# Performance work log

Measured on AMD Instinct MI355X. Metric: run time of the kernel, lower is better.

Reference implementation:

```python
import jax, jax.numpy as jnp
import numpy as np

D_MODEL = 1024
D_STATE = 16
D_CONV = 4
EXPAND = 2
NUM_LAYERS = 2
SEQ = 1024
BATCH = 2
D_INNER = EXPAND * D_MODEL          # 2048
DT_RANK = (D_MODEL + 15) // 16      # 64 (math.ceil(d_model/16))


def setup_inputs() -> dict:
    key = jax.random.key(0)
    ks = jax.random.split(key, 10)
    s = 0.02
    # A initialized as in mamba_ssm: A = repeat(arange(1, d_state+1), d_inner) -> A_log = log(A)
    A_log = jnp.log(jnp.broadcast_to(
        jnp.arange(1, D_STATE + 1, dtype=jnp.float32), (NUM_LAYERS, D_INNER, D_STATE)))
    return {
        "pe": jax.random.normal(ks[0], (SEQ, D_MODEL), jnp.float32) * s,
        "condition": jax.random.normal(ks[1], (BATCH, SEQ, D_MODEL), jnp.float32),
        "W_in": jax.random.normal(ks[2], (NUM_LAYERS, 2 * D_INNER, D_MODEL), jnp.float32) * s,
        "conv_w": jax.random.normal(ks[3], (NUM_LAYERS, D_INNER, D_CONV), jnp.float32) * s,
        "conv_b": jnp.zeros((NUM_LAYERS, D_INNER), jnp.float32),
        "W_x": jax.random.normal(ks[4], (NUM_LAYERS, DT_RANK + 2 * D_STATE, D_INNER), jnp.float32) * s,
        "W_dt": jax.random.normal(ks[5], (NUM_LAYERS, D_INNER, DT_RANK), jnp.float32) * s,
        "b_dt": jax.random.normal(ks[6], (NUM_LAYERS, D_INNER), jnp.float32) * s,
        "A_log": A_log,
        "Dp": jnp.ones((NUM_LAYERS, D_INNER), jnp.float32),
        "W_out": jax.random.normal(ks[7], (NUM_LAYERS, D_MODEL, D_INNER), jnp.float32) * s,
        "output_shape": BATCH,
    }


def _mamba_block(x, W_in, conv_w, conv_b, W_x, W_dt, b_dt, A_log, Dp, W_out):
    # x: [B, L, d_model]
    B, L, _ = x.shape
    xz = jnp.einsum('bld,ed->ble', x, W_in)          # [B, L, 2*d_inner]
    u, z = jnp.split(xz, 2, axis=-1)                 # each [B, L, d_inner]
    # causal depthwise conv1d (padding=d_conv-1, truncate to L)
    xp = jnp.pad(u, ((0, 0), (D_CONV - 1, 0), (0, 0)))
    xc = conv_b + sum(conv_w[:, k] * xp[:, k:k + L, :] for k in range(D_CONV))
    xc = jax.nn.silu(xc)                             # [B, L, d_inner]
    x_dbl = jnp.einsum('bld,ed->ble', xc, W_x)       # [B, L, dt_rank + 2*d_state]
    dt, Bm, Cm = jnp.split(x_dbl, [DT_RANK, DT_RANK + D_STATE], axis=-1)
    delta = jax.nn.softplus(jnp.einsum('blr,dr->bld', dt, W_dt) + b_dt)  # [B, L, d_inner]
    A = -jnp.exp(A_log)                              # [d_inner, d_state]

    def step(h, inputs):
        u_t, d_t, B_t, C_t = inputs                  # [B,di],[B,di],[B,ds],[B,ds]
        dA = jnp.exp(d_t[:, :, None] * A)            # [B, di, ds]
        h = dA * h + (d_t * u_t)[:, :, None] * B_t[:, None, :]
        y = jnp.einsum('bds,bs->bd', h, C_t)
        return h, y

    h0 = jnp.zeros((B, D_INNER, D_STATE), x.dtype)
    xs = (xc.transpose(1, 0, 2), delta.transpose(1, 0, 2),
          Bm.transpose(1, 0, 2), Cm.transpose(1, 0, 2))
    _, ys = jax.lax.scan(step, h0, xs)               # ys: [L, B, d_inner]
    y = ys.transpose(1, 0, 2) + xc * Dp
    out = y * jax.nn.silu(z)
    return jnp.einsum('bld,ed->ble', out, W_out)     # [B, L, d_model]


def reference(pe, condition, W_in, conv_w, conv_b, W_x, W_dt, b_dt, A_log, Dp, W_out, output_shape):
    # pe.repeat(B,1,1) + condition
    x = pe[None, :, :] + condition
    for i in range(NUM_LAYERS):
        x = _mamba_block(x, W_in[i], conv_w[i], conv_b[i], W_x[i],
                         W_dt[i], b_dt[i], A_log[i], Dp[i], W_out[i])
    return x
```

## Files before the change

kernel.cpp:

```cpp
#include <hip/hip_runtime.h>
#include <math.h>

#define D_MODEL 1024
#define D_INNER 2048
#define D_STATE 16
#define DT_RANK 64
#define SEQ 1024
#define BATCH 2
#define NLAYERS 2
#define ROWS (BATCH*SEQ)
#define XDIM 96
#define XZLD (2*D_INNER)

#define NC 32
#define CL 32
#define SDB 256

#define G2_ROWS 64
#define G2_KC 128
#define G2_BK 32
#define G2_KS (D_INNER / G2_KC)

typedef short bf16x8 __attribute__((ext_vector_type(8)));
typedef float f32x4  __attribute__((ext_vector_type(4)));

__device__ __forceinline__ unsigned short f2bf(float f) {
    union { float f; unsigned int u; } v; v.f = f;
    unsigned int u = v.u;
    return (unsigned short)((u + 0x7FFFu + ((u >> 16) & 1u)) >> 16);
}
__device__ __forceinline__ float bf2f(unsigned short u) {
    union { unsigned int i; float f; } v; v.i = ((unsigned int)u) << 16; return v.f;
}

__device__ __forceinline__ void gload_lds16(const void* g, void* s) {
    __builtin_amdgcn_global_load_lds((const __attribute__((address_space(1))) void*)g,
                                     (__attribute__((address_space(3))) void*)s, 16, 0, 0);
}

__global__ __launch_bounds__(256) void add_pe_kernel(const float* __restrict__ pe,
    const float* __restrict__ cond, float* __restrict__ X)
{
    int i = blockIdx.x * 256 + threadIdx.x;
    int total = ROWS * D_MODEL / 4;
    if (i >= total) return;
    int row  = i / (D_MODEL / 4);
    int l    = row & (SEQ - 1);
    int col4 = i - row * (D_MODEL / 4);
    float4 p = reinterpret_cast<const float4*>(pe)[l * (D_MODEL / 4) + col4];
    float4 c = reinterpret_cast<const float4*>(cond)[i];
    float4 r; r.x = p.x + c.x; r.y = p.y + c.y; r.z = p.z + c.z; r.w = p.w + c.w;
    reinterpret_cast<float4*>(X)[i] = r;
}

__global__ __launch_bounds__(256) void add_pe_bf(const float* __restrict__ pe,
    const float* __restrict__ cond, unsigned short* __restrict__ Xbf)
{
    int i = blockIdx.x * 256 + threadIdx.x;
    int total = ROWS * D_MODEL / 4;
    if (i >= total) return;
    int row  = i / (D_MODEL / 4);
    int l    = row & (SEQ - 1);
    int col4 = i - row * (D_MODEL / 4);
    float4 p = reinterpret_cast<const float4*>(pe)[l * (D_MODEL / 4) + col4];
    float4 c = reinterpret_cast<const float4*>(cond)[i];
    ushort4 o;
    o.x = f2bf(p.x + c.x); o.y = f2bf(p.y + c.y);
    o.z = f2bf(p.z + c.z); o.w = f2bf(p.w + c.w);
    reinterpret_cast<ushort4*>(Xbf)[i] = o;
}

__global__ __launch_bounds__(256) void conv_bf16_dense(const float* __restrict__ src,
    unsigned short* __restrict__ dst, int n4)
{
    int i = blockIdx.x * 256 + threadIdx.x;
    if (i >= n4) return;
    float4 v = reinterpret_cast<const float4*>(src)[i];
    ushort4 o; o.x = f2bf(v.x); o.y = f2bf(v.y); o.z = f2bf(v.z); o.w = f2bf(v.w);
    reinterpret_cast<ushort4*>(dst)[i] = o;
}

__global__ __launch_bounds__(256) void conv_bf16_strided(const float* __restrict__ src,
    int ld, int cols, unsigned short* __restrict__ dst, int total4)
{
    int i = blockIdx.x * 256 + threadIdx.x;
    if (i >= total4) return;
    int c4  = cols / 4;
    int row = i / c4;
    int col = (i - row * c4) * 4;
    float4 v = *reinterpret_cast<const float4*>(src + (size_t)row * ld + col);
    ushort4 o; o.x = f2bf(v.x); o.y = f2bf(v.y); o.z = f2bf(v.z); o.w = f2bf(v.w);
    *reinterpret_cast<ushort4*>(dst + (size_t)row * cols + col) = o;
}

__global__ __launch_bounds__(256) void conv_bf16_dtcols(const float* __restrict__ XDBL,
    unsigned short* __restrict__ dst)
{
    int i = blockIdx.x * 256 + threadIdx.x;
    if (i >= ROWS * DT_RANK / 4) return;
    int m  = i >> 4;
    int c4 = (i & 15) * 4;
    float4 v = *reinterpret_cast<const float4*>(XDBL + (size_t)m * XDIM + c4);
    ushort4 o; o.x = f2bf(v.x); o.y = f2bf(v.y); o.z = f2bf(v.z); o.w = f2bf(v.w);
    *reinterpret_cast<ushort4*>(dst + (size_t)m * DT_RANK + c4) = o;
}

#define GBM 128
#define GBN 128
#define GBK 64

#define GEMM_STAGE(Ap, Bp, lda, ldb, koff)                                      \
    _Pragma("unroll")                                                           \
    for (int i_ = 0; i_ < 4; ++i_) {                                            \
        int off_ = w * 4096 + i_ * 1024 + l * 16;                               \
        int row_ = off_ >> 7;                                                   \
        int col_ = (off_ & 127) >> 1;                                           \
        gload_lds16(Ap + (size_t)(m0 + row_) * (lda) + (koff) + col_,           \
                    (char*)As + w * 4096 + i_ * 1024);                          \
    }                                                                           \
    _Pragma("unroll")                                                           \
    for (int i_ = 0; i_ < 4; ++i_) {                                            \
        int off_ = w * 4096 + i_ * 1024 + l * 16;                               \
        int row_ = off_ >> 7;                                                   \
        int col_ = (off_ & 127) >> 1;                                           \
        gload_lds16(Bp + (size_t)(n0 + row_) * (ldb) + (koff) + col_,           \
                    (char*)Bs + w * 4096 + i_ * 1024);                          \
    }

#define GEMM_MFMA_STEP                                                          \
    _Pragma("unroll")                                                           \
    for (int kk = 0; kk < 2; ++kk) {                                            \
        bf16x8 af[4], bfr[4];                                                   \
        _Pragma("unroll")                                                       \
        for (int m = 0; m < 4; ++m)                                             \
            af[m] = *(const bf16x8*)&As[(wr * 64 + m * 16 + fr) * GBK + kk * 32 + fq * 8]; \
        _Pragma("unroll")                                                       \
        for (int n = 0; n < 4; ++n)                                             \
            bfr[n] = *(const bf16x8*)&Bs[(wc * 64 + n * 16 + fr) * GBK + kk * 32 + fq * 8]; \
        _Pragma("unroll")                                                       \
        for (int m = 0; m < 4; ++m)                                             \
            _Pragma("unroll")                                                   \
            for (int n = 0; n < 4; ++n)                                         \
                acc[m][n] = __builtin_amdgcn_mfma_f32_16x16x32_bf16(af[m], bfr[n], acc[m][n], 0, 0, 0); \
    }

__global__ __launch_bounds__(256) void gemm_bf16_nt(const unsigned short* __restrict__ A,
    const unsigned short* __restrict__ B, float* __restrict__ C,
    int M, int N, int K, int ldc, const float* __restrict__ bias, int epilogue)
{
    __shared__ unsigned short As[GBM * GBK];
    __shared__ unsigned short Bs[GBN * GBK];
    int tid = threadIdx.x;
    int w = tid >> 6, l = tid & 63;
    int wr = w >> 1, wc = w & 1;
    int m0 = blockIdx.y * GBM, n0 = blockIdx.x * GBN;

    f32x4 acc[4][4];
    #pragma unroll
    for (int m = 0; m < 4; ++m)
        #pragma unroll
        for (int n = 0; n < 4; ++n) acc[m][n] = (f32x4){0.f, 0.f, 0.f, 0.f};
    int fr = l & 15, fq = l >> 4;

    for (int k0 = 0; k0 < K; k0 += GBK) {
        GEMM_STAGE(A, B, K, K, k0)
        __syncthreads();
        GEMM_MFMA_STEP
        __syncthreads();
    }

    #pragma unroll
    for (int m = 0; m < 4; ++m)
        #pragma unroll
        for (int n = 0; n < 4; ++n) {
            int col = n0 + wc * 64 + n * 16 + fr;
            #pragma unroll
            for (int j = 0; j < 4; ++j) {
                int row = m0 + wr * 64 + m * 16 + fq * 4 + j;
                float v = acc[m][n][j];
                if (epilogue == 1) {
                    v += bias[col];
                    v = fmaxf(v, 0.f) + log1pf(__expf(-fabsf(v)));
                }
                C[(size_t)row * ldc + col] = v;
            }
        }
}

__global__ __launch_bounds__(256) void gemm_bf16_nt_bfout(const unsigned short* __restrict__ A,
    const unsigned short* __restrict__ B, unsigned short* __restrict__ C,
    int M, int N, int K, int ldc)
{
    __shared__ unsigned short As[GBM * GBK];
    __shared__ unsigned short Bs[GBN * GBK];
    int tid = threadIdx.x;
    int w = tid >> 6, l = tid & 63;
    int wr = w >> 1, wc = w & 1;
    int m0 = blockIdx.y * GBM, n0 = blockIdx.x * GBN;

    f32x4 acc[4][4];
    #pragma unroll
    for (int m = 0; m < 4; ++m)
        #pragma unroll
        for (int n = 0; n < 4; ++n) acc[m][n] = (f32x4){0.f, 0.f, 0.f, 0.f};
    int fr = l & 15, fq = l >> 4;

    for (int k0 = 0; k0 < K; k0 += GBK) {
        GEMM_STAGE(A, B, K, K, k0)
        __syncthreads();
        GEMM_MFMA_STEP
        __syncthreads();
    }

    #pragma unroll
    for (int m = 0; m < 4; ++m)
        #pragma unroll
        for (int n = 0; n < 4; ++n) {
            int col = n0 + wc * 64 + n * 16 + fr;
            #pragma unroll
            for (int j = 0; j < 4; ++j) {
                int row = m0 + wr * 64 + m * 16 + fq * 4 + j;
                C[(size_t)row * ldc + col] = f2bf(acc[m][n][j]);
            }
        }
}

__global__ __launch_bounds__(256) void gemm_bf16_sp_bfout(const unsigned short* __restrict__ A,
    const unsigned short* __restrict__ B, unsigned short* __restrict__ C,
    int M, int N, int K, int ldc, const float* __restrict__ bias)
{
    __shared__ unsigned short As[GBM * GBK];
    __shared__ unsigned short Bs[GBN * GBK];
    int tid = threadIdx.x;
    int w = tid >> 6, l = tid & 63;
    int wr = w >> 1, wc = w & 1;
    int m0 = blockIdx.y * GBM, n0 = blockIdx.x * GBN;

    f32x4 acc[4][4];
    #pragma unroll
    for (int m = 0; m < 4; ++m)
        #pragma unroll
        for (int n = 0; n < 4; ++n) acc[m][n] = (f32x4){0.f, 0.f, 0.f, 0.f};
    int fr = l & 15, fq = l >> 4;

    for (int k0 = 0; k0 < K; k0 += GBK) {
        GEMM_STAGE(A, B, K, K, k0)
        __syncthreads();
        GEMM_MFMA_STEP
        __syncthreads();
    }

    #pragma unroll
    for (int m = 0; m < 4; ++m)
        #pragma unroll
        for (int n = 0; n < 4; ++n) {
            int col = n0 + wc * 64 + n * 16 + fr;
            float bv = bias[col];
            #pragma unroll
            for (int j = 0; j < 4; ++j) {
                int row = m0 + wr * 64 + m * 16 + fq * 4 + j;
                float v = acc[m][n][j] + bv;
                v = fmaxf(v, 0.f) + log1pf(__expf(-fabsf(v)));
                C[(size_t)row * ldc + col] = f2bf(v);
            }
        }
}

__global__ __launch_bounds__(256) void gemm_bf16_nt_ks(const unsigned short* __restrict__ A, int lda,
    const unsigned short* __restrict__ B, int ldb, float* __restrict__ P,
    int M, int N, int Kper)
{
    __shared__ unsigned short As[GBM * GBK];
    __shared__ unsigned short Bs[GBN * GBK];
    int tid = threadIdx.x;
    int w = tid >> 6, l = tid & 63;
    int wr = w >> 1, wc = w & 1;
    int m0 = blockIdx.y * GBM, n0 = blockIdx.x * GBN;
    int koff = blockIdx.z * Kper;
    float* Pz = P + (size_t)blockIdx.z * M * N;

    f32x4 acc[4][4];
    #pragma unroll
    for (int m = 0; m < 4; ++m)
        #pragma unroll
        for (int n = 0; n < 4; ++n) acc[m][n] = (f32x4){0.f, 0.f, 0.f, 0.f};
    int fr = l & 15, fq = l >> 4;

    for (int k0 = 0; k0 < Kper; k0 += GBK) {
        GEMM_STAGE(A, B, lda, ldb, koff + k0)
        __syncthreads();
        GEMM_MFMA_STEP
        __syncthreads();
    }

    #pragma unroll
    for (int m = 0; m < 4; ++m)
        #pragma unroll
        for (int n = 0; n < 4; ++n) {
            int col = n0 + wc * 64 + n * 16 + fr;
            #pragma unroll
            for (int j = 0; j < 4; ++j) {
                int row = m0 + wr * 64 + m * 16 + fq * 4 + j;
                Pz[(size_t)row * N + col] = acc[m][n][j];
            }
        }
}

__global__ __launch_bounds__(256) void gemm4_reduce(const float* __restrict__ P,
    float* __restrict__ X, unsigned short* __restrict__ Xbf)
{
    int i = blockIdx.x * 256 + threadIdx.x;
    if (i >= ROWS * D_MODEL / 4) return;
    float4 a = reinterpret_cast<const float4*>(P)[i];
    float4 b = reinterpret_cast<const float4*>(P + (size_t)ROWS * D_MODEL)[i];
    float4 r; r.x = a.x + b.x; r.y = a.y + b.y; r.z = a.z + b.z; r.w = a.w + b.w;
    if (X) reinterpret_cast<float4*>(X)[i] = r;
    if (Xbf) {
        ushort4 o; o.x = f2bf(r.x); o.y = f2bf(r.y); o.z = f2bf(r.z); o.w = f2bf(r.w);
        reinterpret_cast<ushort4*>(Xbf)[i] = o;
    }
}

__global__ __launch_bounds__(256) void gemm2_splitk(const float* __restrict__ A,
    const float* __restrict__ B, float* __restrict__ P)
{
    __shared__ float As[G2_BK][G2_ROWS];
    __shared__ float Bs[G2_BK][XDIM + 1];
    int tid = threadIdx.x;
    int m0 = blockIdx.x * G2_ROWS;
    int kc = blockIdx.y;
    int k0 = kc * G2_KC;

    int rg = tid >> 4;
    int cg = tid & 15;
    float acc[4][6];
    #pragma unroll
    for (int i = 0; i < 4; ++i)
        #pragma unroll
        for (int j = 0; j < 6; ++j) acc[i][j] = 0.f;

    for (int kb = 0; kb < G2_KC; kb += G2_BK) {
        {
            int row = tid & 63;
            int kk  = (tid >> 6) * 4;
            #pragma unroll
            for (int i = 0; i < 2; ++i) {
                float4 v = *(const float4*)(A + (size_t)(m0 + row) * D_INNER + k0 + kb + kk + i * 16);
                As[kk + i * 16 + 0][row] = v.x;
                As[kk + i * 16 + 1][row] = v.y;
                As[kk + i * 16 + 2][row] = v.z;
                As[kk + i * 16 + 3][row] = v.w;
            }
        }
        {
            #pragma unroll
            for (int i = 0; i < 3; ++i) {
                int idx = tid + i * 256;
                int col = idx >> 3;
                int kk  = (idx & 7) * 4;
                float4 v = *(const float4*)(B + (size_t)col * D_INNER + k0 + kb + kk);
                Bs[kk + 0][col] = v.x;
                Bs[kk + 1][col] = v.y;
                Bs[kk + 2][col] = v.z;
                Bs[kk + 3][col] = v.w;
            }
        }
        __syncthreads();
        #pragma unroll
        for (int k = 0; k < G2_BK; ++k) {
            float4 a  = *(const float4*)&As[k][rg * 4];
            float2 b0 = *(const float2*)&Bs[k][cg * 6];
            float2 b1 = *(const float2*)&Bs[k][cg * 6 + 2];
            float2 b2 = *(const float2*)&Bs[k][cg * 6 + 4];
            float av[4] = {a.x, a.y, a.z, a.w};
            float bv[6] = {b0.x, b0.y, b1.x, b1.y, b2.x, b2.y};
            #pragma unroll
            for (int i = 0; i < 4; ++i)
                #pragma unroll
                for (int j = 0; j < 6; ++j) acc[i][j] += av[i] * bv[j];
        }
        __syncthreads();
    }

    #pragma unroll
    for (int i = 0; i < 4; ++i)
        #pragma unroll
        for (int j = 0; j < 6; ++j)
            P[((size_t)kc * ROWS + m0 + rg * 4 + i) * XDIM + cg * 6 + j] = acc[i][j];
}

__global__ __launch_bounds__(256) void gemm2_reduce(const float* __restrict__ P,
    float* __restrict__ XDBLo, unsigned short* __restrict__ dtbf)
{
    int i = blockIdx.x * 256 + threadIdx.x;
    if (i >= ROWS * XDIM / 4) return;
    float4 acc = make_float4(0.f, 0.f, 0.f, 0.f);
    #pragma unroll
    for (int ks = 0; ks < G2_KS; ++ks) {
        float4 v = *(const float4*)(P + (size_t)ks * ROWS * XDIM + (size_t)i * 4);
        acc.x += v.x; acc.y += v.y; acc.z += v.z; acc.w += v.w;
    }
    *(float4*)(XDBLo + (size_t)i * 4) = acc;
    if (dtbf) {
        int row = (i * 4) / XDIM;
        int col = (i * 4) - row * XDIM;
        if (col < DT_RANK) {
            ushort4 o; o.x = f2bf(acc.x); o.y = f2bf(acc.y); o.z = f2bf(acc.z); o.w = f2bf(acc.w);
            *reinterpret_cast<ushort4*>(dtbf + (size_t)row * DT_RANK + col) = o;
        }
    }
}

#define BM 64
#define BN 64
#define BK 16
__global__ __launch_bounds__(256) void gemm_nt(const float* __restrict__ A, int lda,
                                               const float* __restrict__ B, int ldb,
                                               float* __restrict__ C, int ldc,
                                               int M, int N, int K,
                                               const float* __restrict__ bias, int epilogue)
{
    __shared__ float As[BM][BK + 1];
    __shared__ float Bs[BN][BK + 1];
    int t  = threadIdx.x;
    int m0 = blockIdx.y * BM;
    int n0 = blockIdx.x * BN;
    int lrow = t >> 2;
    int lk   = (t & 3) * 4;
    int tm   = t >> 4;
    int tn   = t & 15;

    float acc[4][4];
    #pragma unroll
    for (int i = 0; i < 4; ++i)
        #pragma unroll
        for (int j = 0; j < 4; ++j) acc[i][j] = 0.f;

    for (int k0 = 0; k0 < K; k0 += BK) {
        {
            int row = m0 + lrow;
            float4 v = make_float4(0.f, 0.f, 0.f, 0.f);
            if (row < M) v = *reinterpret_cast<const float4*>(A + (size_t)row * lda + k0 + lk);
            As[lrow][lk + 0] = v.x; As[lrow][lk + 1] = v.y;
            As[lrow][lk + 2] = v.z; As[lrow][lk + 3] = v.w;
        }
        {
            int row = n0 + lrow;
            float4 v = make_float4(0.f, 0.f, 0.f, 0.f);
            if (row < N) v = *reinterpret_cast<const float4*>(B + (size_t)row * ldb + k0 + lk);
            Bs[lrow][lk + 0] = v.x; Bs[lrow][lk + 1] = v.y;
            Bs[lrow][lk + 2] = v.z; Bs[lrow][lk + 3] = v.w;
        }
        __syncthreads();
        #pragma unroll
        for (int kk = 0; kk < BK; ++kk) {
            float a[4], b[4];
            #pragma unroll
            for (int i = 0; i < 4; ++i) a[i] = As[tm * 4 + i][kk];
            #pragma unroll
            for (int j = 0; j < 4; ++j) b[j] = Bs[tn * 4 + j][kk];
            #pragma unroll
            for (int i = 0; i < 4; ++i)
                #pragma unroll
                for (int j = 0; j < 4; ++j) acc[i][j] += a[i] * b[j];
        }
        __syncthreads();
    }

    #pragma unroll
    for (int i = 0; i < 4; ++i) {
        int m = m0 + tm * 4 + i;
        if (m >= M) continue;
        #pragma unroll
        for (int j = 0; j < 4; ++j) {
            int n = n0 + tn * 4 + j;
            if (n >= N) continue;
            float v = acc[i][j];
            if (epilogue == 1) {
                v += bias[n];
                v = fmaxf(v, 0.f) + log1pf(__expf(-fabsf(v)));
            }
            C[(size_t)m * ldc + n] = v;
        }
    }
}

__global__ __launch_bounds__(256) void conv_silu_kernel(const float* __restrict__ XZ,
    const float* __restrict__ cw, const float* __restrict__ cb, float* __restrict__ XC)
{
    int idx = blockIdx.x * 256 + threadIdx.x;
    if (idx >= ROWS * (D_INNER / 4)) return;
    int d4   = idx % (D_INNER / 4);
    int rl   = idx / (D_INNER / 4);
    int l    = rl & (SEQ - 1);
    int base = rl - l;
    int d    = d4 * 4;

    float4 acc = reinterpret_cast<const float4*>(cb)[d4];
    float w[4][4];
    #pragma unroll
    for (int dd = 0; dd < 4; ++dd) {
        float4 wv = *reinterpret_cast<const float4*>(cw + (size_t)(d + dd) * 4);
        w[dd][0] = wv.x; w[dd][1] = wv.y; w[dd][2] = wv.z; w[dd][3] = wv.w;
    }
    #pragma unroll
    for (int k = 0; k < 4; ++k) {
        int lr = l - 3 + k;
        if (lr < 0) continue;
        float4 u = *reinterpret_cast<const float4*>(XZ + (size_t)(base + lr) * XZLD + d);
        acc.x += w[0][k] * u.x; acc.y += w[1][k] * u.y;
        acc.z += w[2][k] * u.z; acc.w += w[3][k] * u.w;
    }
    acc.x = acc.x / (1.f + __expf(-acc.x));
    acc.y = acc.y / (1.f + __expf(-acc.y));
    acc.z = acc.z / (1.f + __expf(-acc.z));
    acc.w = acc.w / (1.f + __expf(-acc.w));
    reinterpret_cast<float4*>(XC)[idx] = acc;
}

__global__ __launch_bounds__(256) void conv_silu_bf(const unsigned short* __restrict__ XZbf,
    const float* __restrict__ cw, const float* __restrict__ cb, float* __restrict__ XC)
{
    int idx = blockIdx.x * 256 + threadIdx.x;
    if (idx >= ROWS * (D_INNER / 4)) return;
    int d4   = idx % (D_INNER / 4);
    int rl   = idx / (D_INNER / 4);
    int l    = rl & (SEQ - 1);
    int base = rl - l;
    int d    = d4 * 4;

    float4 acc = reinterpret_cast<const float4*>(cb)[d4];
    float w[4][4];
    #pragma unroll
    for (int dd = 0; dd < 4; ++dd) {
        float4 wv = *reinterpret_cast<const float4*>(cw + (size_t)(d + dd) * 4);
        w[dd][0] = wv.x; w[dd][1] = wv.y; w[dd][2] = wv.z; w[dd][3] = wv.w;
    }
    #pragma unroll
    for (int k = 0; k < 4; ++k) {
        int lr = l - 3 + k;
        if (lr < 0) continue;
        ushort4 uv = *reinterpret_cast<const ushort4*>(XZbf + (size_t)(base + lr) * XZLD + d);
        acc.x += w[0][k] * bf2f(uv.x); acc.y += w[1][k] * bf2f(uv.y);
        acc.z += w[2][k] * bf2f(uv.z); acc.w += w[3][k] * bf2f(uv.w);
    }
    acc.x = acc.x / (1.f + __expf(-acc.x));
    acc.y = acc.y / (1.f + __expf(-acc.y));
    acc.z = acc.z / (1.f + __expf(-acc.z));
    acc.w = acc.w / (1.f + __expf(-acc.w));
    reinterpret_cast<float4*>(XC)[idx] = acc;
}


__global__ __launch_bounds__(SDB) void scan_part1b(const float* __restrict__ XC,
    const unsigned short* __restrict__ DL, const float* __restrict__ XDBL,
    const float* __restrict__ A_log, float* __restrict__ Psum, float* __restrict__ Ssum)
{
    __shared__ float sB[CL][16];
    int tid = threadIdx.x;
    int d = blockIdx.x * SDB + tid;
    int c = blockIdx.y, b = blockIdx.z;
    size_t r0 = (size_t)b * SEQ + (size_t)c * CL;

    if (tid < CL * 4) {
        int t = tid >> 2, j = (tid & 3) * 4;
        *(float4*)&sB[t][j] = *(const float4*)(XDBL + (r0 + t) * XDIM + DT_RANK + j);
    }

    float a[D_STATE], S[D_STATE];
    #pragma unroll
    for (int i = 0; i < 4; ++i) {
        float4 v = *(const float4*)(A_log + (size_t)d * D_STATE + i * 4);
        a[i*4+0] = -__expf(v.x); a[i*4+1] = -__expf(v.y);
        a[i*4+2] = -__expf(v.z); a[i*4+3] = -__expf(v.w);
    }
    #pragma unroll
    for (int s = 0; s < D_STATE; ++s) S[s] = 0.f;
    float sumdl = 0.f;
    __syncthreads();

    for (int t = 0; t < CL; ++t) {
        float dl = bf2f(DL[(r0 + t) * D_INNER + d]);
        float uu = XC[(r0 + t) * D_INNER + d];
        float du = dl * uu;
        sumdl += dl;
        float4 b0 = *(const float4*)&sB[t][0];
        float4 b1 = *(const float4*)&sB[t][4];
        float4 b2 = *(const float4*)&sB[t][8];
        float4 b3 = *(const float4*)&sB[t][12];
        float bv[16] = {b0.x,b0.y,b0.z,b0.w, b1.x,b1.y,b1.z,b1.w,
                        b2.x,b2.y,b2.z,b2.w, b3.x,b3.y,b3.z,b3.w};
        #pragma unroll
        for (int s = 0; s < D_STATE; ++s) {
            float e = __expf(dl * a[s]);
            S[s] = e * S[s] + du * bv[s];
        }
    }

    size_t o = (((size_t)b * NC + c) * D_INNER + d) * D_STATE;
    #pragma unroll
    for (int i = 0; i < 4; ++i) {
        float4 p, s4;
        p.x = __expf(a[i*4+0] * sumdl); p.y = __expf(a[i*4+1] * sumdl);
        p.z = __expf(a[i*4+2] * sumdl); p.w = __expf(a[i*4+3] * sumdl);
        s4.x = S[i*4+0]; s4.y = S[i*4+1]; s4.z = S[i*4+2]; s4.w = S[i*4+3];
        *(float4*)(Psum + o + i * 4) = p;
        *(float4*)(Ssum + o + i * 4) = s4;
    }
}

__global__ __launch_bounds__(256) void scan_prefix(float* __restrict__ Psum,
    const float* __restrict__ Ssum)
{
    int idx = blockIdx.x * 256 + threadIdx.x;
    int b = idx >> 15;
    int rem = idx & 32767;
    float h = 0.f;
    for (int c = 0; c < NC; ++c) {
        size_t o = (((size_t)b * NC + c) * D_INNER * D_STATE) + rem;
        float p = Psum[o];
        float s = Ssum[o];
        Psum[o] = h;
        h = p * h + s;
    }
}

__global__ __launch_bounds__(SDB) void scan_part2b(const float* __restrict__ XC,
    unsigned short* __restrict__ DL, const unsigned short* __restrict__ XZbf,
    const float* __restrict__ XDBL, const float* __restrict__ A_log,
    const float* __restrict__ Dp, const float* __restrict__ Hin)
{
    __shared__ float sBC[CL][32];
    int tid = threadIdx.x;
    int d = blockIdx.x * SDB + tid;
    int c = blockIdx.y, b = blockIdx.z;
    size_t r0 = (size_t)b * SEQ + (size_t)c * CL;

    {
        int t = tid >> 3, j = (tid & 7) * 4;
        *(float4*)&sBC[t][j] = *(const float4*)(XDBL + (r0 + t) * XDIM + DT_RANK + j);
    }

    float a[D_STATE], h[D_STATE];
    #pragma unroll
    for (int i = 0; i < 4; ++i) {
        float4 v = *(const float4*)(A_log + (size_t)d * D_STATE + i * 4);
        a[i*4+0] = -__expf(v.x); a[i*4+1] = -__expf(v.y);
        a[i*4+2] = -__expf(v.z); a[i*4+3] = -__expf(v.w);
    }
    size_t ho = (((size_t)b * NC + c) * D_INNER + d) * D_STATE;
    #pragma unroll
    for (int i = 0; i < 4; ++i) {
        float4 v = *(const float4*)(Hin + ho + i * 4);
        h[i*4+0] = v.x; h[i*4+1] = v.y; h[i*4+2] = v.z; h[i*4+3] = v.w;
    }
    float dp = Dp[d];
    __syncthreads();

    for (int t = 0; t < CL; ++t) {
        float dl = bf2f(DL[(r0 + t) * D_INNER + d]);
        float uu = XC[(r0 + t) * D_INNER + d];
        float z  = bf2f(XZbf[(r0 + t) * XZLD + D_INNER + d]);
        float du = dl * uu;
        float4 b0 = *(const float4*)&sBC[t][0];
        float4 b1 = *(const float4*)&sBC[t][4];
        float4 b2 = *(const float4*)&sBC[t][8];
        float4 b3 = *(const float4*)&sBC[t][12];
        float4 c0 = *(const float4*)&sBC[t][16];
        float4 c1 = *(const float4*)&sBC[t][20];
        float4 c2 = *(const float4*)&sBC[t][24];
        float4 c3 = *(const float4*)&sBC[t][28];
        float bv[16] = {b0.x,b0.y,b0.z,b0.w, b1.x,b1.y,b1.z,b1.w,
                        b2.x,b2.y,b2.z,b2.w, b3.x,b3.y,b3.z,b3.w};
        float cv[16] = {c0.x,c0.y,c0.z,c0.w, c1.x,c1.y,c1.z,c1.w,
                        c2.x,c2.y,c2.z,c2.w, c3.x,c3.y,c3.z,c3.w};
        float y = 0.f;
        #pragma unroll
        for (int s = 0; s < D_STATE; ++s) {
            float e = __expf(dl * a[s]);
            h[s] = e * h[s] + du * bv[s];
            y += h[s] * cv[s];
        }
        float sz = z / (1.f + __expf(-z));
        DL[(r0 + t) * D_INNER + d] = f2bf((y + uu * dp) * sz);
    }
}

__global__ __launch_bounds__(SDB) void scan_part1(const float* __restrict__ XC,
    const float* __restrict__ XZ, const float* __restrict__ XDBL,
    const float* __restrict__ A_log, float* __restrict__ Psum, float* __restrict__ Ssum)
{
    __shared__ float sB[CL][16];
    int tid = threadIdx.x;
    int d = blockIdx.x * SDB + tid;
    int c = blockIdx.y, b = blockIdx.z;
    size_t r0 = (size_t)b * SEQ + (size_t)c * CL;

    if (tid < CL * 4) {
        int t = tid >> 2, j = (tid & 3) * 4;
        *(float4*)&sB[t][j] = *(const float4*)(XDBL + (r0 + t) * XDIM + DT_RANK + j);
    }

    float a[D_STATE], S[D_STATE];
    #pragma unroll
    for (int i = 0; i < 4; ++i) {
        float4 v = *(const float4*)(A_log + (size_t)d * D_STATE + i * 4);
        a[i*4+0] = -__expf(v.x); a[i*4+1] = -__expf(v.y);
        a[i*4+2] = -__expf(v.z); a[i*4+3] = -__expf(v.w);
    }
    #pragma unroll
    for (int s = 0; s < D_STATE; ++s) S[s] = 0.f;
    float sumdl = 0.f;
    __syncthreads();

    for (int t = 0; t < CL; ++t) {
        float dl = XZ[(r0 + t) * XZLD + d];
        float uu = XC[(r0 + t) * D_INNER + d];
        float du = dl * uu;
        sumdl += dl;
        float4 b0 = *(const float4*)&sB[t][0];
        float4 b1 = *(const float4*)&sB[t][4];
        float4 b2 = *(const float4*)&sB[t][8];
        float4 b3 = *(const float4*)&sB[t][12];
        float bv[16] = {b0.x,b0.y,b0.z,b0.w, b1.x,b1.y,b1.z,b1.w,
                        b2.x,b2.y,b2.z,b2.w, b3.x,b3.y,b3.z,b3.w};
        #pragma unroll
        for (int s = 0; s < D_STATE; ++s) {
            float e = __expf(dl * a[s]);
            S[s] = e * S[s] + du * bv[s];
        }
    }

    size_t o = (((size_t)b * NC + c) * D_INNER + d) * D_STATE;
    #pragma unroll
    for (int i = 0; i < 4; ++i) {
        float4 p, s4;
        p.x = __expf(a[i*4+0] * sumdl); p.y = __expf(a[i*4+1] * sumdl);
        p.z = __expf(a[i*4+2] * sumdl); p.w = __expf(a[i*4+3] * sumdl);
        s4.x = S[i*4+0]; s4.y = S[i*4+1]; s4.z = S[i*4+2]; s4.w = S[i*4+3];
        *(float4*)(Psum + o + i * 4) = p;
        *(float4*)(Ssum + o + i * 4) = s4;
    }
}

__global__ __launch_bounds__(SDB) void scan_part2(const float* __restrict__ XC,
    float* __restrict__ XZ, const float* __restrict__ XDBL,
    const float* __restrict__ A_log, const float* __restrict__ Dp,
    const float* __restrict__ Hin)
{
    __shared__ float sBC[CL][32];
    int tid = threadIdx.x;
    int d = blockIdx.x * SDB + tid;
    int c = blockIdx.y, b = blockIdx.z;
    size_t r0 = (size_t)b * SEQ + (size_t)c * CL;

    {
        int t = tid >> 3, j = (tid & 7) * 4;
        *(float4*)&sBC[t][j] = *(const float4*)(XDBL + (r0 + t) * XDIM + DT_RANK + j);
    }

    float a[D_STATE], h[D_STATE];
    #pragma unroll
    for (int i = 0; i < 4; ++i) {
        float4 v = *(const float4*)(A_log + (size_t)d * D_STATE + i * 4);
        a[i*4+0] = -__expf(v.x); a[i*4+1] = -__expf(v.y);
        a[i*4+2] = -__expf(v.z); a[i*4+3] = -__expf(v.w);
    }
    size_t ho = (((size_t)b * NC + c) * D_INNER + d) * D_STATE;
    #pragma unroll
    for (int i = 0; i < 4; ++i) {
        float4 v = *(const float4*)(Hin + ho + i * 4);
        h[i*4+0] = v.x; h[i*4+1] = v.y; h[i*4+2] = v.z; h[i*4+3] = v.w;
    }
    float dp = Dp[d];
    __syncthreads();

    for (int t = 0; t < CL; ++t) {
        float dl = XZ[(r0 + t) * XZLD + d];
        float uu = XC[(r0 + t) * D_INNER + d];
        float z  = XZ[(r0 + t) * XZLD + D_INNER + d];
        float du = dl * uu;
        float4 b0 = *(const float4*)&sBC[t][0];
        float4 b1 = *(const float4*)&sBC[t][4];
        float4 b2 = *(const float4*)&sBC[t][8];
        float4 b3 = *(const float4*)&sBC[t][12];
        float4 c0 = *(const float4*)&sBC[t][16];
        float4 c1 = *(const float4*)&sBC[t][20];
        float4 c2 = *(const float4*)&sBC[t][24];
        float4 c3 = *(const float4*)&sBC[t][28];
        float bv[16] = {b0.x,b0.y,b0.z,b0.w, b1.x,b1.y,b1.z,b1.w,
                        b2.x,b2.y,b2.z,b2.w, b3.x,b3.y,b3.z,b3.w};
        float cv[16] = {c0.x,c0.y,c0.z,c0.w, c1.x,c1.y,c1.z,c1.w,
                        c2.x,c2.y,c2.z,c2.w, c3.x,c3.y,c3.z,c3.w};
        float y = 0.f;
        #pragma unroll
        for (int s = 0; s < D_STATE; ++s) {
            float e = __expf(dl * a[s]);
            h[s] = e * h[s] + du * bv[s];
            y += h[s] * cv[s];
        }
        float sz = z / (1.f + __expf(-z));
        XZ[(r0 + t) * XZLD + d] = (y + uu * dp) * sz;
    }
}

__global__ __launch_bounds__(256) void scan_kernel2(const float* __restrict__ XC,
    float* __restrict__ XZ, const float* __restrict__ XDBL,
    const float* __restrict__ A_log, const float* __restrict__ Dp)
{
    int tid = threadIdx.x;
    int s  = tid & 15;
    int dd = tid >> 4;
    int d  = blockIdx.x * 16 + dd;
    int b  = blockIdx.y;

    float a  = -__expf(A_log[(size_t)d * D_STATE + s]);
    float h  = 0.f;
    float dp = Dp[d];
    const size_t rbase = (size_t)b * SEQ;

    for (int t = 0; t < SEQ; ++t) {
        size_t r = rbase + t;
        float dl = XZ[r * XZLD + d];
        float uu = XC[r * D_INNER + d];
        float z  = XZ[r * XZLD + D_INNER + d];
        float Bv = XDBL[r * XDIM + DT_RANK + s];
        float Cv = XDBL[r * XDIM + DT_RANK + D_STATE + s];
        float e  = __expf(dl * a);
        h = e * h + dl * uu * Bv;
        float y = h * Cv;
        y += __shfl_xor(y, 1);
        y += __shfl_xor(y, 2);
        y += __shfl_xor(y, 4);
        y += __shfl_xor(y, 8);
        if (s == 0) {
            float sz = z / (1.f + __expf(-z));
            XZ[r * XZLD + d] = (y + uu * dp) * sz;
        }
    }
}

extern "C" void kernel_launch(void* const* d_in, const int* in_sizes, int n_in,
                              void* d_out, int out_size, void* d_ws, size_t ws_size,
                              hipStream_t stream)
{
    const float* pe    = (const float*)d_in[0];
    const float* cond  = (const float*)d_in[1];
    const float* W_in  = (const float*)d_in[2];
    const float* cw    = (const float*)d_in[3];
    const float* cb    = (const float*)d_in[4];
    const float* W_x   = (const float*)d_in[5];
    const float* W_dt  = (const float*)d_in[6];
    const float* b_dt  = (const float*)d_in[7];
    const float* A_log = (const float*)d_in[8];
    const float* Dp    = (const float*)d_in[9];
    const float* W_out = (const float*)d_in[10];

    float* X = (float*)d_out;

    char* wsp = (char*)d_ws;
    unsigned short* XZbf = (unsigned short*)wsp;
    float* XC    = (float*)(wsp + 16777216);
    float* XDBL  = (float*)(wsp + 33554432);
    unsigned short* BF0   = (unsigned short*)(wsp + 34340864);
    unsigned short* dtbf  = (unsigned short*)(wsp + 42729472);
    unsigned short* WINbf = (unsigned short*)(wsp + 42991616);
    unsigned short* WOUTbf= (unsigned short*)(wsp + 59768832);
    unsigned short* WDTbf = (unsigned short*)(wsp + 68157440);
    float* SCR   = (float*)(wsp + 68681728);
    size_t need_A = 68681728 + 16777216;

    float* XZb   = (float*)d_ws;
    float* XCb   = XZb + (size_t)ROWS * XZLD;
    float* XDBLb = XCb + (size_t)ROWS * D_INNER;
    void* rest = (void*)(XDBLb + (size_t)ROWS * XDIM);
    unsigned short* Abf = (unsigned short*)rest;
    unsigned short* Bbf = Abf + (size_t)ROWS * D_INNER;
    float* PpartB = (float*)rest;
    float* PsumB  = (float*)rest;
    float* SsumB  = PsumB + (size_t)BATCH * NC * D_INNER * D_STATE;
    size_t need_B = ((size_t)ROWS * XZLD + (size_t)ROWS * D_INNER + (size_t)ROWS * XDIM) * 4
                  + ((size_t)ROWS * D_INNER + (size_t)ROWS * D_INNER) * 2;

    if (ws_size >= need_A) {
        float* Psum = SCR;
        float* Ssum = SCR + (size_t)BATCH * NC * D_INNER * D_STATE;

        conv_bf16_dense<<<(NLAYERS * 2 * D_INNER * D_MODEL / 4 + 255) / 256, 256, 0, stream>>>(
            W_in, WINbf, NLAYERS * 2 * D_INNER * D_MODEL / 4);
        conv_bf16_dense<<<(NLAYERS * D_MODEL * D_INNER / 4 + 255) / 256, 256, 0, stream>>>(
            W_out, WOUTbf, NLAYERS * D_MODEL * D_INNER / 4);
        conv_bf16_dense<<<(NLAYERS * D_INNER * DT_RANK / 4 + 255) / 256, 256, 0, stream>>>(
            W_dt, WDTbf, NLAYERS * D_INNER * DT_RANK / 4);
        add_pe_bf<<<ROWS * D_MODEL / 4 / 256, 256, 0, stream>>>(pe, cond, BF0);

        for (int l = 0; l < NLAYERS; ++l) {
            const unsigned short* WINl  = WINbf  + (size_t)l * 2 * D_INNER * D_MODEL;
            const unsigned short* WOUTl = WOUTbf + (size_t)l * D_MODEL * D_INNER;
            const unsigned short* WDTl  = WDTbf  + (size_t)l * D_INNER * DT_RANK;
            const float* W_x_l   = W_x   + (size_t)l * XDIM * D_INNER;
            const float* b_dt_l  = b_dt  + (size_t)l * D_INNER;
            const float* A_log_l = A_log + (size_t)l * D_INNER * D_STATE;
            const float* Dp_l    = Dp    + (size_t)l * D_INNER;

            gemm_bf16_nt_bfout<<<dim3(2 * D_INNER / GBN, ROWS / GBM), 256, 0, stream>>>(
                BF0, WINl, XZbf, ROWS, 2 * D_INNER, D_MODEL, XZLD);
            conv_silu_bf<<<ROWS * (D_INNER / 4) / 256, 256, 0, stream>>>(
                XZbf, cw + (size_t)l * D_INNER * 4, cb + (size_t)l * D_INNER, XC);
            gemm2_splitk<<<dim3(ROWS / G2_ROWS, G2_KS), 256, 0, stream>>>(XC, W_x_l, SCR);
            gemm2_reduce<<<(ROWS * XDIM / 4 + 255) / 256, 256, 0, stream>>>(SCR, XDBL, dtbf);
            gemm_bf16_sp_bfout<<<dim3(D_INNER / GBN, ROWS / GBM), 256, 0, stream>>>(
                dtbf, WDTl, BF0, ROWS, D_INNER, DT_RANK, D_INNER, b_dt_l);
            scan_part1b<<<dim3(D_INNER / SDB, NC, BATCH), SDB, 0, stream>>>(
                XC, BF0, XDBL, A_log_l, Psum, Ssum);
            scan_prefix<<<BATCH * D_INNER * D_STATE / 256, 256, 0, stream>>>(Psum, Ssum);
            scan_part2b<<<dim3(D_INNER / SDB, NC, BATCH), SDB, 0, stream>>>(
                XC, BF0, XZbf, XDBL, A_log_l, Dp_l, Psum);
            gemm_bf16_nt_ks<<<dim3(D_MODEL / GBN, ROWS / GBM, 2), 256, 0, stream>>>(
                BF0, D_INNER, WOUTl, D_INNER, SCR, ROWS, D_MODEL, D_INNER / 2);
            gemm4_reduce<<<(ROWS * D_MODEL / 4 + 255) / 256, 256, 0, stream>>>(
                SCR, (l == NLAYERS - 1) ? X : nullptr, (l < NLAYERS - 1) ? BF0 : nullptr);
        }
    } else if (ws_size >= need_B) {
        add_pe_kernel<<<ROWS * D_MODEL / 4 / 256, 256, 0, stream>>>(pe, cond, X);
        for (int l = 0; l < NLAYERS; ++l) {
            const float* W_in_l  = W_in  + (size_t)l * 2 * D_INNER * D_MODEL;
            const float* W_out_l = W_out + (size_t)l * D_MODEL * D_INNER;
            const float* W_x_l   = W_x   + (size_t)l * XDIM * D_INNER;
            const float* W_dt_l  = W_dt  + (size_t)l * D_INNER * DT_RANK;
            const float* b_dt_l  = b_dt  + (size_t)l * D_INNER;
            const float* A_log_l = A_log + (size_t)l * D_INNER * D_STATE;
            const float* Dp_l    = Dp    + (size_t)l * D_INNER;

            conv_bf16_dense<<<(ROWS * D_MODEL / 4 + 255) / 256, 256, 0, stream>>>(X, Abf, ROWS * D_MODEL / 4);
            conv_bf16_dense<<<(2 * D_INNER * D_MODEL / 4 + 255) / 256, 256, 0, stream>>>(W_in_l, Bbf, 2 * D_INNER * D_MODEL / 4);
            gemm_bf16_nt<<<dim3(2 * D_INNER / GBN, ROWS / GBM), 256, 0, stream>>>(
                Abf, Bbf, XZb, ROWS, 2 * D_INNER, D_MODEL, XZLD, nullptr, 0);
            conv_silu_kernel<<<ROWS * (D_INNER / 4) / 256, 256, 0, stream>>>(
                XZb, cw + (size_t)l * D_INNER * 4, cb + (size_t)l * D_INNER, XCb);
            gemm2_splitk<<<dim3(ROWS / G2_ROWS, G2_KS), 256, 0, stream>>>(XCb, W_x_l, PpartB);
            gemm2_reduce<<<(ROWS * XDIM / 4 + 255) / 256, 256, 0, stream>>>(PpartB, XDBLb, nullptr);
            conv_bf16_dtcols<<<(ROWS * DT_RANK / 4 + 255) / 256, 256, 0, stream>>>(XDBLb, Abf);
            conv_bf16_dense<<<(D_INNER * DT_RANK / 4 + 255) / 256, 256, 0, stream>>>(W_dt_l, Bbf, D_INNER * DT_RANK / 4);
            gemm_bf16_nt<<<dim3(D_INNER / GBN, ROWS / GBM), 256, 0, stream>>>(
                Abf, Bbf, XZb, ROWS, D_INNER, DT_RANK, XZLD, b_dt_l, 1);
            scan_part1<<<dim3(D_INNER / SDB, NC, BATCH), SDB, 0, stream>>>(
                XCb, XZb, XDBLb, A_log_l, PsumB, SsumB);
            scan_prefix<<<BATCH * D_INNER * D_STATE / 256, 256, 0, stream>>>(PsumB, SsumB);
            scan_part2<<<dim3(D_INNER / SDB, NC, BATCH), SDB, 0, stream>>>(
                XCb, XZb, XDBLb, A_log_l, Dp_l, PsumB);
            conv_bf16_strided<<<(ROWS * D_INNER / 4 + 255) / 256, 256, 0, stream>>>(
                XZb, XZLD, D_INNER, Abf, ROWS * D_INNER / 4);
            conv_bf16_dense<<<(D_MODEL * D_INNER / 4 + 255) / 256, 256, 0, stream>>>(W_out_l, Bbf, D_MODEL * D_INNER / 4);
            gemm_bf16_nt<<<dim3(D_MODEL / GBN, ROWS / GBM), 256, 0, stream>>>(
                Abf, Bbf, X, ROWS, D_MODEL, D_INNER, D_MODEL, nullptr, 0);
        }
    } else {
        add_pe_kernel<<<ROWS * D_MODEL / 4 / 256, 256, 0, stream>>>(pe, cond, X);
        for (int l = 0; l < NLAYERS; ++l) {
            gemm_nt<<<dim3(2 * D_INNER / BN, ROWS / BM), 256, 0, stream>>>(
                X, D_MODEL, W_in + (size_t)l * 2 * D_INNER * D_MODEL, D_MODEL,
                XZb, XZLD, ROWS, 2 * D_INNER, D_MODEL, nullptr, 0);
            conv_silu_kernel<<<ROWS * (D_INNER / 4) / 256, 256, 0, stream>>>(
                XZb, cw + (size_t)l * D_INNER * 4, cb + (size_t)l * D_INNER, XCb);
            gemm_nt<<<dim3((XDIM + BN - 1) / BN, ROWS / BM), 256, 0, stream>>>(
                XCb, D_INNER, W_x + (size_t)l * XDIM * D_INNER, D_INNER,
                XDBLb, XDIM, ROWS, XDIM, D_INNER, nullptr, 0);
            gemm_nt<<<dim3(D_INNER / BN, ROWS / BM), 256, 0, stream>>>(
                XDBLb, XDIM, W_dt + (size_t)l * D_INNER * DT_RANK, DT_RANK,
                XZb, XZLD, ROWS, D_INNER, DT_RANK, b_dt + (size_t)l * D_INNER, 1);
            scan_kernel2<<<dim3(D_INNER / 16, BATCH), 256, 0, stream>>>(
                XCb, XZb, XDBLb, A_log + (size_t)l * D_INNER * D_STATE, Dp + (size_t)l * D_INNER);
            gemm_nt<<<dim3(D_MODEL / BN, ROWS / BM), 256, 0, stream>>>(
                XZb, XZLD, W_out + (size_t)l * D_MODEL * D_INNER, D_INNER,
                X, D_MODEL, ROWS, D_MODEL, D_INNER, nullptr, 0);
        }
    }
}
```

Measured before the change: 381.6 us.

## Fuse causal conv+SiLU into x_proj split-K GEMM, store xc as bf16

The depthwise causal conv and SiLU are now computed inside the x_proj split-K GEMM. Each block builds its A tile in shared memory straight from the bf16 XZ buffer and also writes a bf16 copy of xc for the scan kernels, which replaces the separate conv kernel and its fp32 XC round trip. The three weight-conversion launches are merged into one kernel. In exchange the scans read xc at reduced precision, and the fused conv loads are strided scalar reads along the sequence, which may coalesce poorly.

```diff
diff --git a/kernel.cpp b/kernel.cpp
--- a/kernel.cpp
+++ b/kernel.cpp
@@ -78,6 +78,25 @@
     float4 v = reinterpret_cast<const float4*>(src)[i];
     ushort4 o; o.x = f2bf(v.x); o.y = f2bf(v.y); o.z = f2bf(v.z); o.w = f2bf(v.w);
     reinterpret_cast<ushort4*>(dst)[i] = o;
+}
+
+#define WN1 (NLAYERS * 2 * D_INNER * D_MODEL / 4)
+#define WN2 (NLAYERS * D_MODEL * D_INNER / 4)
+#define WN3 (NLAYERS * D_INNER * DT_RANK / 4)
+__global__ __launch_bounds__(256) void conv_wall(const float* __restrict__ Win,
+    const float* __restrict__ Wout, const float* __restrict__ Wdt,
+    unsigned short* __restrict__ WINbf, unsigned short* __restrict__ WOUTbf,
+    unsigned short* __restrict__ WDTbf)
+{
+    int i = blockIdx.x * 256 + threadIdx.x;
+    const float* src; unsigned short* dst; int j;
+    if (i < WN1)              { src = Win;  dst = WINbf;  j = i; }
+    else if (i < WN1 + WN2)   { src = Wout; dst = WOUTbf; j = i - WN1; }
+    else if (i < WN1+WN2+WN3) { src = Wdt;  dst = WDTbf;  j = i - WN1 - WN2; }
+    else return;
+    float4 v = reinterpret_cast<const float4*>(src)[j];
+    ushort4 o; o.x = f2bf(v.x); o.y = f2bf(v.y); o.z = f2bf(v.z); o.w = f2bf(v.w);
+    reinterpret_cast<ushort4*>(dst)[j] = o;
 }
 
 __global__ __launch_bounds__(256) void conv_bf16_strided(const float* __restrict__ src,
@@ -321,16 +340,41 @@
     }
 }
 
-__global__ __launch_bounds__(256) void gemm2_splitk(const float* __restrict__ A,
-    const float* __restrict__ B, float* __restrict__ P)
-{
-    __shared__ float As[G2_BK][G2_ROWS];
+__global__ __launch_bounds__(256) void gemm2_fused(const unsigned short* __restrict__ XZbf,
+    const float* __restrict__ cw, const float* __restrict__ cb,
+    const float* __restrict__ B, unsigned short* __restrict__ XCbf,
+    float* __restrict__ P)
+{
+    __shared__ float Axc[G2_KC][68];
     __shared__ float Bs[G2_BK][XDIM + 1];
     int tid = threadIdx.x;
     int m0 = blockIdx.x * G2_ROWS;
     int kc = blockIdx.y;
     int k0 = kc * G2_KC;
 
+    {
+        int d_loc = tid & 127;
+        int d     = k0 + d_loc;
+        int r0    = m0 + (tid >> 7) * 32;
+        float4 wv = *(const float4*)(cw + (size_t)d * 4);
+        float cbv = cb[d];
+        int l0 = r0 & (SEQ - 1);
+        float u3 = (l0 >= 3) ? bf2f(XZbf[(size_t)(r0 - 3) * XZLD + d]) : 0.f;
+        float u2 = (l0 >= 2) ? bf2f(XZbf[(size_t)(r0 - 2) * XZLD + d]) : 0.f;
+        float u1 = (l0 >= 1) ? bf2f(XZbf[(size_t)(r0 - 1) * XZLD + d]) : 0.f;
+        int rl0 = r0 - m0;
+        #pragma unroll 4
+        for (int t = 0; t < 32; ++t) {
+            float u0 = bf2f(XZbf[(size_t)(r0 + t) * XZLD + d]);
+            float v = cbv + wv.x * u3 + wv.y * u2 + wv.z * u1 + wv.w * u0;
+            v = v / (1.f + __expf(-v));
+            Axc[d_loc][rl0 + t] = v;
+            XCbf[(size_t)(r0 + t) * D_INNER + d] = f2bf(v);
+            u3 = u2; u2 = u1; u1 = u0;
+        }
+    }
+    __syncthreads();
+
     int rg = tid >> 4;
     int cg = tid & 15;
     float acc[4][6];
@@ -340,18 +384,6 @@
         for (int j = 0; j < 6; ++j) acc[i][j] = 0.f;
 
     for (int kb = 0; kb < G2_KC; kb += G2_BK) {
-        {
-            int row = tid & 63;
-            int kk  = (tid >> 6) * 4;
-            #pragma unroll
-            for (int i = 0; i < 2; ++i) {
-                float4 v = *(const float4*)(A + (size_t)(m0 + row) * D_INNER + k0 + kb + kk + i * 16);
-                As[kk + i * 16 + 0][row] = v.x;
-                As[kk + i * 16 + 1][row] = v.y;
-                As[kk + i * 16 + 2][row] = v.z;
-                As[kk + i * 16 + 3][row] = v.w;
-            }
-        }
         {
             #pragma unroll
             for (int i = 0; i < 3; ++i) {
@@ -368,6 +400,74 @@
         __syncthreads();
         #pragma unroll
         for (int k = 0; k < G2_BK; ++k) {
+            float4 a  = *(const float4*)&Axc[kb + k][rg * 4];
+            float2 b0 = *(const float2*)&Bs[k][cg * 6];
+            float2 b1 = *(const float2*)&Bs[k][cg * 6 + 2];
+            float2 b2 = *(const float2*)&Bs[k][cg * 6 + 4];
+            float av[4] = {a.x, a.y, a.z, a.w};
+            float bv[6] = {b0.x, b0.y, b1.x, b1.y, b2.x, b2.y};
+            #pragma unroll
+            for (int i = 0; i < 4; ++i)
+                #pragma unroll
+                for (int j = 0; j < 6; ++j) acc[i][j] += av[i] * bv[j];
+        }
+        __syncthreads();
+    }
+
+    #pragma unroll
+    for (int i = 0; i < 4; ++i)
+        #pragma unroll
+        for (int j = 0; j < 6; ++j)
+            P[((size_t)kc * ROWS + m0 + rg * 4 + i) * XDIM + cg * 6 + j] = acc[i][j];
+}
+
+__global__ __launch_bounds__(256) void gemm2_splitk(const float* __restrict__ A,
+    const float* __restrict__ B, float* __restrict__ P)
+{
+    __shared__ float As[G2_BK][G2_ROWS];
+    __shared__ float Bs[G2_BK][XDIM + 1];
+    int tid = threadIdx.x;
+    int m0 = blockIdx.x * G2_ROWS;
+    int kc = blockIdx.y;
+    int k0 = kc * G2_KC;
+
+    int rg = tid >> 4;
+    int cg = tid & 15;
+    float acc[4][6];
+    #pragma unroll
+    for (int i = 0; i < 4; ++i)
+        #pragma unroll
+        for (int j = 0; j < 6; ++j) acc[i][j] = 0.f;
+
+    for (int kb = 0; kb < G2_KC; kb += G2_BK) {
+        {
+            int row = tid & 63;
+            int kk  = (tid >> 6) * 4;
+            #pragma unroll
+            for (int i = 0; i < 2; ++i) {
+                float4 v = *(const float4*)(A + (size_t)(m0 + row) * D_INNER + k0 + kb + kk + i * 16);
+                As[kk + i * 16 + 0][row] = v.x;
+                As[kk + i * 16 + 1][row] = v.y;
+                As[kk + i * 16 + 2][row] = v.z;
+                As[kk + i * 16 + 3][row] = v.w;
+            }
+        }
+        {
+            #pragma unroll
+            for (int i = 0; i < 3; ++i) {
+                int idx = tid + i * 256;
+                int col = idx >> 3;
+                int kk  = (idx & 7) * 4;
+                float4 v = *(const float4*)(B + (size_t)col * D_INNER + k0 + kb + kk);
+                Bs[kk + 0][col] = v.x;
+                Bs[kk + 1][col] = v.y;
+                Bs[kk + 2][col] = v.z;
+                Bs[kk + 3][col] = v.w;
+            }
+        }
+        __syncthreads();
+        #pragma unroll
+        for (int k = 0; k < G2_BK; ++k) {
             float4 a  = *(const float4*)&As[k][rg * 4];
             float2 b0 = *(const float2*)&Bs[k][cg * 6];
             float2 b1 = *(const float2*)&Bs[k][cg * 6 + 2];
@@ -518,41 +618,8 @@
     reinterpret_cast<float4*>(XC)[idx] = acc;
 }
 
-__global__ __launch_bounds__(256) void conv_silu_bf(const unsigned short* __restrict__ XZbf,
-    const float* __restrict__ cw, const float* __restrict__ cb, float* __restrict__ XC)
-{
-    int idx = blockIdx.x * 256 + threadIdx.x;
-    if (idx >= ROWS * (D_INNER / 4)) return;
-    int d4   = idx % (D_INNER / 4);
-    int rl   = idx / (D_INNER / 4);
-    int l    = rl & (SEQ - 1);
-    int base = rl - l;
-    int d    = d4 * 4;
-
-    float4 acc = reinterpret_cast<const float4*>(cb)[d4];
-    float w[4][4];
-    #pragma unroll
-    for (int dd = 0; dd < 4; ++dd) {
-        float4 wv = *reinterpret_cast<const float4*>(cw + (size_t)(d + dd) * 4);
-        w[dd][0] = wv.x; w[dd][1] = wv.y; w[dd][2] = wv.z; w[dd][3] = wv.w;
-    }
-    #pragma unroll
-    for (int k = 0; k < 4; ++k) {
-        int lr = l - 3 + k;
-        if (lr < 0) continue;
-        ushort4 uv = *reinterpret_cast<const ushort4*>(XZbf + (size_t)(base + lr) * XZLD + d);
-        acc.x += w[0][k] * bf2f(uv.x); acc.y += w[1][k] * bf2f(uv.y);
-        acc.z += w[2][k] * bf2f(uv.z); acc.w += w[3][k] * bf2f(uv.w);
-    }
-    acc.x = acc.x / (1.f + __expf(-acc.x));
-    acc.y = acc.y / (1.f + __expf(-acc.y));
-    acc.z = acc.z / (1.f + __expf(-acc.z));
-    acc.w = acc.w / (1.f + __expf(-acc.w));
-    reinterpret_cast<float4*>(XC)[idx] = acc;
-}
-
-
-__global__ __launch_bounds__(SDB) void scan_part1b(const float* __restrict__ XC,
+
+__global__ __launch_bounds__(SDB) void scan_part1b(const unsigned short* __restrict__ XCbf,
     const unsigned short* __restrict__ DL, const float* __restrict__ XDBL,
     const float* __restrict__ A_log, float* __restrict__ Psum, float* __restrict__ Ssum)
 {
@@ -581,7 +648,7 @@
 
     for (int t = 0; t < CL; ++t) {
         float dl = bf2f(DL[(r0 + t) * D_INNER + d]);
-        float uu = XC[(r0 + t) * D_INNER + d];
+        float uu = bf2f(XCbf[(r0 + t) * D_INNER + d]);
         float du = dl * uu;
         sumdl += dl;
         float4 b0 = *(const float4*)&sB[t][0];
@@ -625,7 +692,7 @@
     }
 }
 
-__global__ __launch_bounds__(SDB) void scan_part2b(const float* __restrict__ XC,
+__global__ __launch_bounds__(SDB) void scan_part2b(const unsigned short* __restrict__ XCbf,
     unsigned short* __restrict__ DL, const unsigned short* __restrict__ XZbf,
     const float* __restrict__ XDBL, const float* __restrict__ A_log,
     const float* __restrict__ Dp, const float* __restrict__ Hin)
@@ -659,7 +726,7 @@
 
     for (int t = 0; t < CL; ++t) {
         float dl = bf2f(DL[(r0 + t) * D_INNER + d]);
-        float uu = XC[(r0 + t) * D_INNER + d];
+        float uu = bf2f(XCbf[(r0 + t) * D_INNER + d]);
         float z  = bf2f(XZbf[(r0 + t) * XZLD + D_INNER + d]);
         float du = dl * uu;
         float4 b0 = *(const float4*)&sBC[t][0];
@@ -860,7 +927,7 @@
 
     char* wsp = (char*)d_ws;
     unsigned short* XZbf = (unsigned short*)wsp;
-    float* XC    = (float*)(wsp + 16777216);
+    unsigned short* XCbf = (unsigned short*)(wsp + 16777216);
     float* XDBL  = (float*)(wsp + 33554432);
     unsigned short* BF0   = (unsigned short*)(wsp + 34340864);
     unsigned short* dtbf  = (unsigned short*)(wsp + 42729472);
@@ -886,12 +953,8 @@
         float* Psum = SCR;
         float* Ssum = SCR + (size_t)BATCH * NC * D_INNER * D_STATE;
 
-        conv_bf16_dense<<<(NLAYERS * 2 * D_INNER * D_MODEL / 4 + 255) / 256, 256, 0, stream>>>(
-            W_in, WINbf, NLAYERS * 2 * D_INNER * D_MODEL / 4);
-        conv_bf16_dense<<<(NLAYERS * D_MODEL * D_INNER / 4 + 255) / 256, 256, 0, stream>>>(
-            W_out, WOUTbf, NLAYERS * D_MODEL * D_INNER / 4);
-        conv_bf16_dense<<<(NLAYERS * D_INNER * DT_RANK / 4 + 255) / 256, 256, 0, stream>>>(
-            W_dt, WDTbf, NLAYERS * D_INNER * DT_RANK / 4);
+        conv_wall<<<(WN1 + WN2 + WN3 + 255) / 256, 256, 0, stream>>>(
+            W_in, W_out, W_dt, WINbf, WOUTbf, WDTbf);
         add_pe_bf<<<ROWS * D_MODEL / 4 / 256, 256, 0, stream>>>(pe, cond, BF0);
 
         for (int l = 0; l < NLAYERS; ++l) {
@@ -905,17 +968,17 @@
 
             gemm_bf16_nt_bfout<<<dim3(2 * D_INNER / GBN, ROWS / GBM), 256, 0, stream>>>(
                 BF0, WINl, XZbf, ROWS, 2 * D_INNER, D_MODEL, XZLD);
-            conv_silu_bf<<<ROWS * (D_INNER / 4) / 256, 256, 0, stream>>>(
-                XZbf, cw + (size_t)l * D_INNER * 4, cb + (size_t)l * D_INNER, XC);
-            gemm2_splitk<<<dim3(ROWS / G2_ROWS, G2_KS), 256, 0, stream>>>(XC, W_x_l, SCR);
+            gemm2_fused<<<dim3(ROWS / G2_ROWS, G2_KS), 256, 0, stream>>>(
+                XZbf, cw + (size_t)l * D_INNER * 4, cb + (size_t)l * D_INNER,
+                W_x_l, XCbf, SCR);
             gemm2_reduce<<<(ROWS * XDIM / 4 + 255) / 256, 256, 0, stream>>>(SCR, XDBL, dtbf);
             gemm_bf16_sp_bfout<<<dim3(D_INNER / GBN, ROWS / GBM), 256, 0, stream>>>(
                 dtbf, WDTl, BF0, ROWS, D_INNER, DT_RANK, D_INNER, b_dt_l);
             scan_part1b<<<dim3(D_INNER / SDB, NC, BATCH), SDB, 0, stream>>>(
-                XC, BF0, XDBL, A_log_l, Psum, Ssum);
+                XCbf, BF0, XDBL, A_log_l, Psum, Ssum);
             scan_prefix<<<BATCH * D_INNER * D_STATE / 256, 256, 0, stream>>>(Psum, Ssum);
             scan_part2b<<<dim3(D_INNER / SDB, NC, BATCH), SDB, 0, stream>>>(
-                XC, BF0, XZbf, XDBL, A_log_l, Dp_l, Psum);
+                XCbf, BF0, XZbf, XDBL, A_log_l, Dp_l, Psum);
             gemm_bf16_nt_ks<<<dim3(D_MODEL / GBN, ROWS / GBM, 2), 256, 0, stream>>>(
                 BF0, D_INNER, WOUTl, D_INNER, SCR, ROWS, D_MODEL, D_INNER / 2);
             gemm4_reduce<<<(ROWS * D_MODEL / 4 + 255) / 256, 256, 0, stream>>>(
```

Result: faster. 342.6 us (-10.2%).
